# Optimization experiments

Hardware: AMD Instinct MI355X
Metric: run time of the kernel (lower is better)

## Reference

```python
import jax, jax.numpy as jnp
import numpy as np

B, C, F = 16384, 1000, 256
ALPHA = 10


def setup_inputs() -> dict:
    key = jax.random.key(0)
    k1, k2, k3, k4, k5 = jax.random.split(key, 5)
    logits = jax.random.normal(k1, (B, C), dtype=jnp.float32)
    features = jax.random.normal(k2, (B, F), dtype=jnp.float32)
    mean_vecs = jax.random.normal(k3, (C, F), dtype=jnp.float32)
    # Per-class Weibull (shape, loc, scale) as fit by scipy.weibull_min.fit.
    wb_shape = jax.random.uniform(k4, (C,), dtype=jnp.float32, minval=1.0, maxval=4.0)
    wb_loc = jnp.zeros((C,), dtype=jnp.float32)
    # typical tail distance for randn features/means is ~sqrt(2F) ~ 22.6
    wb_scale = jax.random.uniform(k5, (C,), dtype=jnp.float32, minval=10.0, maxval=25.0)
    return {"logits": logits, "features": features, "mean_vecs": mean_vecs,
            "wb_shape": wb_shape, "wb_loc": wb_loc, "wb_scale": wb_scale}


def reference(logits, features, mean_vecs, wb_shape, wb_loc, wb_scale):
    # Batched per-class Euclidean distances via the GEMM identity
    # ||f - m||^2 = ||f||^2 + ||m||^2 - 2 f.m  (avoids [B,C,F] intermediate).
    f2 = jnp.sum(features * features, axis=1, keepdims=True)        # [B,1]
    m2 = jnp.sum(mean_vecs * mean_vecs, axis=1)                     # [C]
    d2 = f2 + m2[None, :] - 2.0 * (features @ mean_vecs.T)          # [B,C]
    dist = jnp.sqrt(jnp.maximum(d2, 1e-12))                         # [B,C]
    # Analytic weibull_min CDF: 1 - exp(-((x - loc)/scale)^c), 0 for x <= loc.
    xp = (dist - wb_loc[None, :]) / wb_scale[None, :]
    pos = xp > 0
    xp_safe = jnp.where(pos, xp, 1.0)
    w = jnp.where(pos, 1.0 - jnp.exp(-(xp_safe ** wb_shape[None, :])), 0.0)
    # OpenMax reweighting + softmax (exp/sum-normalize as in the original).
    scores = logits * (1.0 - w ** ALPHA)                            # [B,C]
    return jax.nn.softmax(scores, axis=-1)
```

## Files before the change

kernel.cpp:

```cpp
#include <hip/hip_runtime.h>

#define NB 16384
#define NC 1000
#define NF 256
#define SE_STRIDE 1004

typedef _Float16 half8 __attribute__((ext_vector_type(8)));
typedef float f32x4 __attribute__((ext_vector_type(4)));

__global__ __launch_bounds__(256) void prep_kernel(
    const float* __restrict__ mean_vecs,
    const float* __restrict__ wb_shape,
    const float* __restrict__ wb_loc,
    const float* __restrict__ wb_scale,
    _Float16* __restrict__ m16f,
    float* __restrict__ pm2,
    float* __restrict__ psh,
    float* __restrict__ pli,
    float* __restrict__ pis)
{
    const int lane = threadIdx.x & 63;
    const int W = blockIdx.x * 4 + (threadIdx.x >> 6);

    if (W < 512) {
        const int gt = W >> 3, kk = W & 7;
        int cls = gt * 16 + (lane & 15);
        if (cls > NC - 1) cls = NC - 1;
        const float* src = mean_vecs + (size_t)cls * NF + kk * 32 + (lane >> 4) * 8;
        const float4 lo = *(const float4*)src;
        const float4 hi = *(const float4*)(src + 4);
        half8 h;
        h[0]=(_Float16)lo.x; h[1]=(_Float16)lo.y; h[2]=(_Float16)lo.z; h[3]=(_Float16)lo.w;
        h[4]=(_Float16)hi.x; h[5]=(_Float16)hi.y; h[6]=(_Float16)hi.z; h[7]=(_Float16)hi.w;
        *((half8*)m16f + (size_t)W * 64 + lane) = h;
    }
    if (W < NC) {
        const float4 v = *((const float4*)(mean_vecs + (size_t)W * NF) + lane);
        float s = v.x*v.x + v.y*v.y + v.z*v.z + v.w*v.w;
        #pragma unroll
        for (int off = 1; off < 64; off <<= 1) s += __shfl_xor(s, off, 64);
        if (lane == 0) {
            const float isc = 1.0f / wb_scale[W];
            pm2[W] = s;
            psh[W] = wb_shape[W];
            pli[W] = wb_loc[W] * isc;
            pis[W] = isc;
        }
    }
}

__global__ __launch_bounds__(512, 4) void score_kernel(
    const float* __restrict__ logits,
    const float* __restrict__ features,
    const _Float16* __restrict__ m16f,
    const float* __restrict__ pm2,
    const float* __restrict__ psh,
    const float* __restrict__ pli,
    const float* __restrict__ pis,
    float* __restrict__ out)
{
    __shared__ float se[16][SE_STRIDE];
    __shared__ float ssum[8][16];
    __shared__ float sinv[16];

    const int lane = threadIdx.x & 63;
    const int wave = threadIdx.x >> 6;
    const int q    = lane >> 4;
    const int mr   = lane & 15;
    const int row  = blockIdx.x * 16 + mr;

    half8 bfrag[8];
    float f2 = 0.f;
    const float* fb = features + (size_t)row * NF;
    #pragma unroll
    for (int kk = 0; kk < 8; ++kk) {
        const float4* p = (const float4*)(fb + kk * 32 + q * 8);
        const float4 lo = p[0], hi = p[1];
        f2 += lo.x*lo.x + lo.y*lo.y + lo.z*lo.z + lo.w*lo.w
            + hi.x*hi.x + hi.y*hi.y + hi.z*hi.z + hi.w*hi.w;
        half8 b;
        b[0]=(_Float16)lo.x; b[1]=(_Float16)lo.y; b[2]=(_Float16)lo.z; b[3]=(_Float16)lo.w;
        b[4]=(_Float16)hi.x; b[5]=(_Float16)hi.y; b[6]=(_Float16)hi.z; b[7]=(_Float16)hi.w;
        bfrag[kk] = b;
    }
    f2 += __shfl_xor(f2, 16, 64);
    f2 += __shfl_xor(f2, 32, 64);

    const float LOG2E = 1.44269504088896340736f;
    float rsum = 0.f;

    const half8* mbase = (const half8*)m16f + (size_t)(wave * 8) * 8 * 64 + lane;
    const float* lrow  = logits + (size_t)row * NC;

    half8 a[8];
    #pragma unroll
    for (int kk = 0; kk < 8; ++kk)
        a[kk] = mbase[kk * 64];
    float4 lg = *(const float4*)(lrow + (wave * 128 + q * 4));

    #pragma unroll
    for (int t = 0; t < 8; ++t) {
        const int gt   = wave * 8 + t;
        const int cb   = gt * 16 + q * 4;
        const bool cvg = (cb <= NC - 4);
        const int cbc  = cvg ? cb : (NC - 4);

        f32x4 acc = {0.f, 0.f, 0.f, 0.f};
        #pragma unroll
        for (int kk = 0; kk < 8; ++kk)
            acc = __builtin_amdgcn_mfma_f32_16x16x32_f16(a[kk], bfrag[kk], acc, 0, 0, 0);

        float4 lgn = lg;
        if (t < 7) {
            #pragma unroll
            for (int kk = 0; kk < 8; ++kk)
                a[kk] = mbase[(size_t)((t + 1) * 8 + kk) * 64];
            const int cbn  = cb + 16;
            const int cbnc = (cbn <= NC - 4) ? cbn : (NC - 4);
            lgn = *(const float4*)(lrow + cbnc);
        }

        const float4 m2v = *(const float4*)(pm2 + cbc);
        const float4 shv = *(const float4*)(psh + cbc);
        const float4 liv = *(const float4*)(pli + cbc);
        const float4 iv  = *(const float4*)(pis + cbc);

        const float* m2a = (const float*)&m2v;
        const float* sha = (const float*)&shv;
        const float* lia = (const float*)&liv;
        const float* iva = (const float*)&iv;
        const float* lga = (const float*)&lg;

        f32x4 o;
        #pragma unroll
        for (int j = 0; j < 4; ++j) {
            float d2   = fmaxf(f2 + m2a[j] - 2.0f * acc[j], 1e-12f);
            float dist = sqrtf(d2);
            float xp   = dist * iva[j] - lia[j];
            float xs   = fmaxf(xp, 1e-30f);
            float tt   = exp2f(sha[j] * log2f(xs));
            float w    = 1.0f - exp2f(-LOG2E * tt);
            w = (xp > 0.f) ? w : 0.f;
            float w2 = w * w, w4 = w2 * w2, w8 = w4 * w4;
            float s  = lga[j] * (1.0f - w8 * w2);
            float e  = exp2f(LOG2E * s);
            e = cvg ? e : 0.f;
            rsum += e;
            o[j] = e;
        }

        if (cvg)
            *(f32x4*)&se[mr][cb] = o;

        lg = lgn;
    }

    rsum += __shfl_xor(rsum, 16, 64);
    rsum += __shfl_xor(rsum, 32, 64);
    if (lane < 16) ssum[wave][lane] = rsum;
    __syncthreads();
    if (wave == 0 && lane < 16) {
        float tot = 0.f;
        #pragma unroll
        for (int w = 0; w < 8; ++w) tot += ssum[w][lane];
        sinv[lane] = 1.0f / tot;
    }
    __syncthreads();

    #pragma unroll
    for (int rr = 0; rr < 2; ++rr) {
        const int r = wave * 2 + rr;
        const float inv = sinv[r];
        float* orow = out + (size_t)(blockIdx.x * 16 + r) * NC;
        #pragma unroll
        for (int i = 0; i < 4; ++i) {
            const int idx = i * 64 + lane;
            if (idx < 250) {
                float4 v = *(const float4*)&se[r][idx * 4];
                v.x *= inv; v.y *= inv; v.z *= inv; v.w *= inv;
                *(float4*)(orow + idx * 4) = v;
            }
        }
    }
}

extern "C" void kernel_launch(void* const* d_in, const int* in_sizes, int n_in,
                              void* d_out, int out_size, void* d_ws, size_t ws_size,
                              hipStream_t stream) {
    const float* logits    = (const float*)d_in[0];
    const float* features  = (const float*)d_in[1];
    const float* mean_vecs = (const float*)d_in[2];
    const float* wb_shape  = (const float*)d_in[3];
    const float* wb_loc    = (const float*)d_in[4];
    const float* wb_scale  = (const float*)d_in[5];
    float* out = (float*)d_out;

    _Float16* m16f = (_Float16*)d_ws;
    float* pm2 = (float*)((char*)d_ws + 524288);
    float* psh = (float*)((char*)d_ws + 524288 + 4096);
    float* pli = (float*)((char*)d_ws + 524288 + 8192);
    float* pis = (float*)((char*)d_ws + 524288 + 12288);

    prep_kernel<<<252, 256, 0, stream>>>(mean_vecs, wb_shape, wb_loc, wb_scale,
                                         m16f, pm2, psh, pli, pis);
    score_kernel<<<NB / 16, 512, 0, stream>>>(logits, features, m16f,
                                              pm2, psh, pli, pis, out);
}
```

Before: 183.7 us.

## Move logits load and exp into row-wise softmax epilogue with coalesced reads

Phase 1 now stores only the Weibull gain factor (1 - w^10) into shared memory and no longer reads logits per MFMA fragment. The epilogue has each wave own two rows: it reads logits with coalesced float4 loads, computes the exp, and reduces the row sum with a wave shuffle, which removes one block barrier and the cross-wave ssum/sinv shared arrays. The mean-vector fragment loads are also hoisted ahead of the feature loads. The aim is better-coalesced logits traffic and less synchronisation, at the cost of serialising the logits load after the GEMM phase instead of prefetching it.

```diff
diff --git a/kernel.cpp b/kernel.cpp
--- a/kernel.cpp
+++ b/kernel.cpp
@@ -60,14 +60,19 @@
     float* __restrict__ out)
 {
     __shared__ float se[16][SE_STRIDE];
-    __shared__ float ssum[8][16];
-    __shared__ float sinv[16];
 
     const int lane = threadIdx.x & 63;
     const int wave = threadIdx.x >> 6;
     const int q    = lane >> 4;
     const int mr   = lane & 15;
     const int row  = blockIdx.x * 16 + mr;
+
+    const half8* mbase = (const half8*)m16f + (size_t)(wave * 8) * 8 * 64 + lane;
+
+    half8 a[8];
+    #pragma unroll
+    for (int kk = 0; kk < 8; ++kk)
+        a[kk] = mbase[kk * 64];
 
     half8 bfrag[8];
     float f2 = 0.f;
@@ -87,16 +92,6 @@
     f2 += __shfl_xor(f2, 32, 64);
 
     const float LOG2E = 1.44269504088896340736f;
-    float rsum = 0.f;
-
-    const half8* mbase = (const half8*)m16f + (size_t)(wave * 8) * 8 * 64 + lane;
-    const float* lrow  = logits + (size_t)row * NC;
-
-    half8 a[8];
-    #pragma unroll
-    for (int kk = 0; kk < 8; ++kk)
-        a[kk] = mbase[kk * 64];
-    float4 lg = *(const float4*)(lrow + (wave * 128 + q * 4));
 
     #pragma unroll
     for (int t = 0; t < 8; ++t) {
@@ -110,14 +105,10 @@
         for (int kk = 0; kk < 8; ++kk)
             acc = __builtin_amdgcn_mfma_f32_16x16x32_f16(a[kk], bfrag[kk], acc, 0, 0, 0);
 
-        float4 lgn = lg;
         if (t < 7) {
             #pragma unroll
             for (int kk = 0; kk < 8; ++kk)
                 a[kk] = mbase[(size_t)((t + 1) * 8 + kk) * 64];
-            const int cbn  = cb + 16;
-            const int cbnc = (cbn <= NC - 4) ? cbn : (NC - 4);
-            lgn = *(const float4*)(lrow + cbnc);
         }
 
         const float4 m2v = *(const float4*)(pm2 + cbc);
@@ -129,7 +120,6 @@
         const float* sha = (const float*)&shv;
         const float* lia = (const float*)&liv;
         const float* iva = (const float*)&iv;
-        const float* lga = (const float*)&lg;
 
         f32x4 o;
         #pragma unroll
@@ -142,41 +132,49 @@
             float w    = 1.0f - exp2f(-LOG2E * tt);
             w = (xp > 0.f) ? w : 0.f;
             float w2 = w * w, w4 = w2 * w2, w8 = w4 * w4;
-            float s  = lga[j] * (1.0f - w8 * w2);
-            float e  = exp2f(LOG2E * s);
-            e = cvg ? e : 0.f;
-            rsum += e;
-            o[j] = e;
+            o[j] = 1.0f - w8 * w2;
         }
 
         if (cvg)
             *(f32x4*)&se[mr][cb] = o;
-
-        lg = lgn;
-    }
-
-    rsum += __shfl_xor(rsum, 16, 64);
-    rsum += __shfl_xor(rsum, 32, 64);
-    if (lane < 16) ssum[wave][lane] = rsum;
-    __syncthreads();
-    if (wave == 0 && lane < 16) {
-        float tot = 0.f;
-        #pragma unroll
-        for (int w = 0; w < 8; ++w) tot += ssum[w][lane];
-        sinv[lane] = 1.0f / tot;
-    }
+    }
+
     __syncthreads();
 
     #pragma unroll
     for (int rr = 0; rr < 2; ++rr) {
         const int r = wave * 2 + rr;
-        const float inv = sinv[r];
-        float* orow = out + (size_t)(blockIdx.x * 16 + r) * NC;
+        const size_t grow = (size_t)(blockIdx.x * 16 + r);
+        const float* lrow = logits + grow * NC;
+
+        float4 ev[4];
+        float psum = 0.f;
         #pragma unroll
         for (int i = 0; i < 4; ++i) {
             const int idx = i * 64 + lane;
             if (idx < 250) {
-                float4 v = *(const float4*)&se[r][idx * 4];
+                const float4 g4 = *(const float4*)&se[r][idx * 4];
+                const float4 l4 = *(const float4*)(lrow + idx * 4);
+                float4 e4;
+                e4.x = exp2f(LOG2E * (l4.x * g4.x));
+                e4.y = exp2f(LOG2E * (l4.y * g4.y));
+                e4.z = exp2f(LOG2E * (l4.z * g4.z));
+                e4.w = exp2f(LOG2E * (l4.w * g4.w));
+                ev[i] = e4;
+                psum += (e4.x + e4.y) + (e4.z + e4.w);
+            }
+        }
+        #pragma unroll
+        for (int off = 1; off < 64; off <<= 1)
+            psum += __shfl_xor(psum, off, 64);
+        const float inv = 1.0f / psum;
+
+        float* orow = out + grow * NC;
+        #pragma unroll
+        for (int i = 0; i < 4; ++i) {
+            const int idx = i * 64 + lane;
+            if (idx < 250) {
+                float4 v = ev[i];
                 v.x *= inv; v.y *= inv; v.z *= inv; v.w *= inv;
                 *(float4*)(orow + idx * 4) = v;
             }
```

Result: faster. 170.8 us (-7.0%).
